# Kernel tuning notes

Hardware: AMD Instinct MI355X
Metric: run time of the kernel (lower is better)

## Reference

```python
import jax, jax.numpy as jnp
import numpy as np

DIM = 192
WH, WW = 8, 8
N = WH * WW
NUM_HEADS = 6
HEAD_DIM = DIM // NUM_HEADS
SCALE = HEAD_DIM ** (-0.5)
B_ = 4096


def _relative_position_index(Wh, Ww):
    coords = np.stack(np.meshgrid(np.arange(Wh), np.arange(Ww), indexing='ij'))  # [2, Wh, Ww]
    cf = coords.reshape(2, -1)                              # [2, N]
    rel = cf[:, :, None] - cf[:, None, :]                   # [2, N, N]
    rel = rel.transpose(1, 2, 0).astype(np.int64)           # [N, N, 2]
    rel[..., 0] += Wh - 1
    rel[..., 1] += Ww - 1
    rel[..., 0] *= 2 * Ww - 1
    return rel.sum(-1)                                      # [N, N]


REL_IDX = jnp.asarray(_relative_position_index(WH, WW))


def setup_inputs() -> dict:
    key = jax.random.key(0)
    ks = jax.random.split(key, 6)
    x = jax.random.normal(ks[0], (B_, N, DIM), dtype=jnp.float32)
    w_qkv = jax.random.normal(ks[1], (3 * DIM, DIM), dtype=jnp.float32) * (DIM ** -0.5)
    b_qkv = jnp.zeros((3 * DIM,), dtype=jnp.float32)
    w_proj = jax.random.normal(ks[2], (DIM, DIM), dtype=jnp.float32) * (DIM ** -0.5)
    b_proj = jnp.zeros((DIM,), dtype=jnp.float32)
    # torch init is zeros; use small noise so the bias path is exercised
    bias_table = jax.random.normal(ks[3], ((2 * WH - 1) * (2 * WW - 1), NUM_HEADS), dtype=jnp.float32) * 0.02
    return {"x": x, "w_qkv": w_qkv, "b_qkv": b_qkv, "w_proj": w_proj,
            "b_proj": b_proj, "bias_table": bias_table}


def reference(x, w_qkv, b_qkv, w_proj, b_proj, bias_table):
    B, n, C = x.shape
    qkv = jnp.einsum('bnc,dc->bnd', x, w_qkv) + b_qkv        # [B, N, 3C]
    qkv = qkv.reshape(B, n, 3, NUM_HEADS, HEAD_DIM)
    q = qkv[:, :, 0].transpose(0, 2, 1, 3) * SCALE            # [B, H, N, hd]
    k = qkv[:, :, 1].transpose(0, 2, 1, 3)
    v = qkv[:, :, 2].transpose(0, 2, 1, 3)
    attn = jnp.einsum('bhnd,bhmd->bhnm', q, k)                # [B, H, N, N]
    bias = bias_table[REL_IDX]                                # [N, N, H]
    attn = attn + bias.transpose(2, 0, 1)[None]               # broadcast over B
    attn = jax.nn.softmax(attn, axis=-1)
    out = jnp.einsum('bhnm,bhmd->bnhd', attn, v).reshape(B, n, C)
    return jnp.einsum('bnc,dc->bnd', out, w_proj) + b_proj
```

## Files before the change

### kernel.cpp

```cpp
#include <hip/hip_runtime.h>

#define TOK 64
#define CDIM 192
#define NH 6
#define HD 32
#define NWAVE 12
#define THREADS 768
#define QSCALE 0.17677669529663687f
#define W16_BYTES ((110592 + 36864) * 2)

typedef _Float16 f16x8 __attribute__((ext_vector_type(8)));
typedef _Float16 f16x4 __attribute__((ext_vector_type(4)));
typedef float f32x4 __attribute__((ext_vector_type(4)));

__device__ __forceinline__ f16x8 ld8(const _Float16* p) {
  return *reinterpret_cast<const f16x8*>(p);
}

__device__ __forceinline__ f16x8 cvt8(const float* __restrict__ p) {
  float4 a = *reinterpret_cast<const float4*>(p);
  float4 c = *reinterpret_cast<const float4*>(p + 4);
  f16x8 r;
  r[0] = (_Float16)a.x; r[1] = (_Float16)a.y; r[2] = (_Float16)a.z; r[3] = (_Float16)a.w;
  r[4] = (_Float16)c.x; r[5] = (_Float16)c.y; r[6] = (_Float16)c.z; r[7] = (_Float16)c.w;
  return r;
}

__global__ void cvt_weights(const float* __restrict__ wq, const float* __restrict__ wp,
                            _Float16* __restrict__ w16) {
  int i = blockIdx.x * 256 + threadIdx.x;
  if (i < 27648) {
    float4 v = reinterpret_cast<const float4*>(wq)[i];
    f16x4 h;
    h[0] = (_Float16)v.x; h[1] = (_Float16)v.y; h[2] = (_Float16)v.z; h[3] = (_Float16)v.w;
    *reinterpret_cast<f16x4*>(w16 + (size_t)i * 4) = h;
  } else if (i < 36864) {
    int j = i - 27648;
    float4 v = reinterpret_cast<const float4*>(wp)[j];
    f16x4 h;
    h[0] = (_Float16)v.x; h[1] = (_Float16)v.y; h[2] = (_Float16)v.z; h[3] = (_Float16)v.w;
    *reinterpret_cast<f16x4*>(w16 + 110592 + (size_t)j * 4) = h;
  }
}

template <bool W16>
__global__ __launch_bounds__(THREADS, 1) void winattn(
    const float* __restrict__ x, const float* __restrict__ w_qkv,
    const float* __restrict__ b_qkv, const float* __restrict__ w_proj,
    const float* __restrict__ b_proj, const float* __restrict__ bias_table,
    const _Float16* __restrict__ w16, float* __restrict__ out) {
  __shared__ __align__(16) _Float16 xob[24 * TOK * 8];
  __shared__ __align__(16) _Float16 qb[NH * 4 * TOK * 8];
  __shared__ __align__(16) _Float16 kb[NH * 4 * TOK * 8];
  __shared__ __align__(16) _Float16 vtb[NH * 8 * HD * 8];
  __shared__ __align__(16) _Float16 pbw[NWAVE * 16 * TOK];
  __shared__ float bias_sm[225 * NH];

  const int tid = threadIdx.x;
  const int w   = tid >> 6;
  const int l   = tid & 63;
  const int l15 = l & 15;
  const int lg  = l >> 4;
  const int b   = blockIdx.x;
  const f32x4 vzero = {0.f, 0.f, 0.f, 0.f};

  const float* xg = x + (size_t)b * (TOK * CDIM);
#pragma unroll
  for (int i = tid; i < TOK * CDIM / 4; i += THREADS) {
    int n = i / (CDIM / 4);
    int c = (i % (CDIM / 4)) * 4;
    float4 v = reinterpret_cast<const float4*>(xg)[i];
    f16x4 h4;
    h4[0] = (_Float16)v.x; h4[1] = (_Float16)v.y;
    h4[2] = (_Float16)v.z; h4[3] = (_Float16)v.w;
    *reinterpret_cast<f16x4*>(&xob[((c >> 3) * TOK + n) * 8 + (c & 7)]) = h4;
  }
  for (int i = tid; i < 225 * NH; i += THREADS) bias_sm[i] = bias_table[i];
  __syncthreads();

  const int h   = w >> 1;
  const int sdl = h * HD + (w & 1) * 16 + l15;
  f32x4 acc[3][4];
#pragma unroll
  for (int p = 0; p < 3; ++p)
#pragma unroll
    for (int mt = 0; mt < 4; ++mt) acc[p][mt] = vzero;

#pragma unroll
  for (int ks = 0; ks < 6; ++ks) {
    f16x8 a[4];
#pragma unroll
    for (int mt = 0; mt < 4; ++mt)
      a[mt] = ld8(&xob[((ks * 4 + lg) * TOK + mt * 16 + l15) * 8]);
#pragma unroll
    for (int p = 0; p < 3; ++p) {
      int row = p * CDIM + sdl;
      f16x8 bf;
      if constexpr (W16) bf = ld8(w16 + (size_t)row * CDIM + ks * 32 + lg * 8);
      else               bf = cvt8(w_qkv + (size_t)row * CDIM + ks * 32 + lg * 8);
#pragma unroll
      for (int mt = 0; mt < 4; ++mt)
        acc[p][mt] = __builtin_amdgcn_mfma_f32_16x16x32_f16(a[mt], bf, acc[p][mt], 0, 0, 0);
    }
  }
  {
    const int hd = (w & 1) * 16 + l15;
    float bq0 = b_qkv[sdl], bq1 = b_qkv[CDIM + sdl], bq2 = b_qkv[2 * CDIM + sdl];
#pragma unroll
    for (int mt = 0; mt < 4; ++mt) {
#pragma unroll
      for (int r = 0; r < 4; ++r) {
        int n = mt * 16 + lg * 4 + r;
        qb[h * 2048 + ((hd >> 3) * TOK + n) * 8 + (hd & 7)] =
            (_Float16)((acc[0][mt][r] + bq0) * QSCALE);
        kb[h * 2048 + ((hd >> 3) * TOK + n) * 8 + (hd & 7)] =
            (_Float16)(acc[1][mt][r] + bq1);
        vtb[h * 2048 + ((n >> 3) * HD + hd) * 8 + (n & 7)] =
            (_Float16)(acc[2][mt][r] + bq2);
      }
    }
  }
  __syncthreads();

  {
    const int pw = w * (16 * TOK);
#pragma unroll
    for (int ii = 0; ii < 2; ++ii) {
      const int it = (w & 1) * 2 + ii;
      f16x8 qf = ld8(&qb[h * 2048 + (lg * TOK + it * 16 + l15) * 8]);
      f32x4 st[4];
#pragma unroll
      for (int jt = 0; jt < 4; ++jt) {
        f16x8 kf = ld8(&kb[h * 2048 + (lg * TOK + jt * 16 + l15) * 8]);
        st[jt] = __builtin_amdgcn_mfma_f32_16x16x32_f16(kf, qf, vzero, 0, 0, 0);
      }
      const int i = it * 16 + l15, yi = i >> 3, xi = i & 7;
#pragma unroll
      for (int jt = 0; jt < 4; ++jt) {
#pragma unroll
        for (int r = 0; r < 4; ++r) {
          int j = jt * 16 + lg * 4 + r, yj = j >> 3, xj = j & 7;
          st[jt][r] += bias_sm[((yi - yj + 7) * 15 + (xi - xj + 7)) * NH + h];
        }
      }
      float m = st[0][0];
#pragma unroll
      for (int jt = 0; jt < 4; ++jt)
#pragma unroll
        for (int r = 0; r < 4; ++r) m = fmaxf(m, st[jt][r]);
      m = fmaxf(m, __shfl_xor(m, 16, 64));
      m = fmaxf(m, __shfl_xor(m, 32, 64));
      float e[4][4], sum = 0.f;
#pragma unroll
      for (int jt = 0; jt < 4; ++jt)
#pragma unroll
        for (int r = 0; r < 4; ++r) { e[jt][r] = __expf(st[jt][r] - m); sum += e[jt][r]; }
      sum += __shfl_xor(sum, 16, 64);
      sum += __shfl_xor(sum, 32, 64);
      float inv = 1.f / sum;
#pragma unroll
      for (int jt = 0; jt < 4; ++jt) {
        f16x4 pk;
#pragma unroll
        for (int r = 0; r < 4; ++r) pk[r] = (_Float16)(e[jt][r] * inv);
        *reinterpret_cast<f16x4*>(
            &pbw[pw + ((jt * 2 + (lg >> 1)) * 16 + l15) * 8 + (lg & 1) * 4]) = pk;
      }
      f32x4 o[2] = {vzero, vzero};
#pragma unroll
      for (int ks = 0; ks < 2; ++ks) {
        f16x8 pf = ld8(&pbw[pw + ((ks * 4 + lg) * 16 + l15) * 8]);
#pragma unroll
        for (int nt = 0; nt < 2; ++nt) {
          f16x8 vf = ld8(&vtb[h * 2048 + ((ks * 4 + lg) * HD + nt * 16 + l15) * 8]);
          o[nt] = __builtin_amdgcn_mfma_f32_16x16x32_f16(pf, vf, o[nt], 0, 0, 0);
        }
      }
#pragma unroll
      for (int nt = 0; nt < 2; ++nt) {
        int c = h * HD + nt * 16 + l15;
#pragma unroll
        for (int r = 0; r < 4; ++r) {
          int i2 = it * 16 + lg * 4 + r;
          xob[((c >> 3) * TOK + i2) * 8 + (c & 7)] = (_Float16)o[nt][r];
        }
      }
    }
  }
  __syncthreads();

  {
    const int e = w * 16 + l15;
    f32x4 pacc[4];
#pragma unroll
    for (int mt = 0; mt < 4; ++mt) pacc[mt] = vzero;
#pragma unroll
    for (int ks = 0; ks < 6; ++ks) {
      f16x8 bf;
      if constexpr (W16) bf = ld8(w16 + 110592 + (size_t)e * CDIM + ks * 32 + lg * 8);
      else               bf = cvt8(w_proj + (size_t)e * CDIM + ks * 32 + lg * 8);
#pragma unroll
      for (int mt = 0; mt < 4; ++mt) {
        f16x8 a = ld8(&xob[((ks * 4 + lg) * TOK + mt * 16 + l15) * 8]);
        pacc[mt] = __builtin_amdgcn_mfma_f32_16x16x32_f16(a, bf, pacc[mt], 0, 0, 0);
      }
    }
    float bp = b_proj[e];
#pragma unroll
    for (int mt = 0; mt < 4; ++mt) {
#pragma unroll
      for (int r = 0; r < 4; ++r) {
        int n = mt * 16 + lg * 4 + r;
        out[((size_t)b * TOK + n) * CDIM + e] = pacc[mt][r] + bp;
      }
    }
  }
}

extern "C" void kernel_launch(void* const* d_in, const int* in_sizes, int n_in,
                              void* d_out, int out_size, void* d_ws, size_t ws_size,
                              hipStream_t stream) {
  const float* x          = (const float*)d_in[0];
  const float* w_qkv      = (const float*)d_in[1];
  const float* b_qkv      = (const float*)d_in[2];
  const float* w_proj     = (const float*)d_in[3];
  const float* b_proj     = (const float*)d_in[4];
  const float* bias_table = (const float*)d_in[5];
  float* out = (float*)d_out;
  int B = in_sizes[0] / (TOK * CDIM);

  if (ws_size >= (size_t)W16_BYTES) {
    _Float16* w16 = (_Float16*)d_ws;
    hipLaunchKernelGGL(cvt_weights, dim3(144), dim3(256), 0, stream, w_qkv, w_proj, w16);
    hipLaunchKernelGGL(winattn<true>, dim3(B), dim3(THREADS), 0, stream,
                       x, w_qkv, b_qkv, w_proj, b_proj, bias_table, w16, out);
  } else {
    hipLaunchKernelGGL(winattn<false>, dim3(B), dim3(THREADS), 0, stream,
                       x, w_qkv, b_qkv, w_proj, b_proj, bias_table,
                       (const _Float16*)nullptr, out);
  }
}
```

Baseline: 266.6 us.

## Halve block to six waves, reuse LDS buffers, precompute per-lane bias layout

The block shrinks from 12 to 6 waves, one wave per head, and launch bounds now request three blocks per CU. LDS drops to three reused 24 KB buffers so more blocks fit. The prep kernel also expands the relative-position bias into a per-lane fp16 layout in workspace, replacing per-element shared-memory gather and index arithmetic with two vector loads. Each wave carries more accumulators (6x4 tiles), which raises register pressure, and an extra barrier is added to allow buffer reuse.

Result: slower. 323.3 us (+21.3%).

```diff
diff --git a/kernel.cpp b/kernel.cpp
--- a/kernel.cpp
+++ b/kernel.cpp
@@ -4,10 +4,15 @@
 #define CDIM 192
 #define NH 6
 #define HD 32
-#define NWAVE 12
-#define THREADS 768
+#define NWAVE 6
+#define THREADS 384
 #define QSCALE 0.17677669529663687f
-#define W16_BYTES ((110592 + 36864) * 2)
+
+#define WQ16_OFF 0
+#define WP16_OFF 110592
+#define BIAS_OFF 147456
+#define WS_HALFS (147456 + 24576)
+#define WS_BYTES (WS_HALFS * 2)
 
 typedef _Float16 f16x8 __attribute__((ext_vector_type(8)));
 typedef _Float16 f16x4 __attribute__((ext_vector_type(4)));
@@ -26,34 +31,42 @@
   return r;
 }
 
-__global__ void cvt_weights(const float* __restrict__ wq, const float* __restrict__ wp,
-                            _Float16* __restrict__ w16) {
+__global__ void prep_ws(const float* __restrict__ wq, const float* __restrict__ wp,
+                        const float* __restrict__ bt, _Float16* __restrict__ ws) {
   int i = blockIdx.x * 256 + threadIdx.x;
   if (i < 27648) {
     float4 v = reinterpret_cast<const float4*>(wq)[i];
     f16x4 h;
     h[0] = (_Float16)v.x; h[1] = (_Float16)v.y; h[2] = (_Float16)v.z; h[3] = (_Float16)v.w;
-    *reinterpret_cast<f16x4*>(w16 + (size_t)i * 4) = h;
+    *reinterpret_cast<f16x4*>(ws + WQ16_OFF + (size_t)i * 4) = h;
   } else if (i < 36864) {
     int j = i - 27648;
     float4 v = reinterpret_cast<const float4*>(wp)[j];
     f16x4 h;
     h[0] = (_Float16)v.x; h[1] = (_Float16)v.y; h[2] = (_Float16)v.z; h[3] = (_Float16)v.w;
-    *reinterpret_cast<f16x4*>(w16 + 110592 + (size_t)j * 4) = h;
-  }
-}
-
-template <bool W16>
-__global__ __launch_bounds__(THREADS, 1) void winattn(
+    *reinterpret_cast<f16x4*>(ws + WP16_OFF + (size_t)j * 4) = h;
+  } else if (i < 61440) {
+    int j = i - 36864;
+    int hit = j >> 10;
+    int l = (j >> 4) & 63;
+    int s = j & 15;
+    int h = hit >> 2, it = hit & 3;
+    int ii = it * 16 + (l & 15);
+    int jj = (s >> 2) * 16 + (l >> 4) * 4 + (s & 3);
+    int rel = ((ii >> 3) - (jj >> 3) + 7) * 15 + ((ii & 7) - (jj & 7) + 7);
+    ws[BIAS_OFF + j] = (_Float16)bt[rel * NH + h];
+  }
+}
+
+template <bool WS>
+__global__ __launch_bounds__(THREADS, 3) void winattn(
     const float* __restrict__ x, const float* __restrict__ w_qkv,
     const float* __restrict__ b_qkv, const float* __restrict__ w_proj,
     const float* __restrict__ b_proj, const float* __restrict__ bias_table,
-    const _Float16* __restrict__ w16, float* __restrict__ out) {
-  __shared__ __align__(16) _Float16 xob[24 * TOK * 8];
-  __shared__ __align__(16) _Float16 qb[NH * 4 * TOK * 8];
-  __shared__ __align__(16) _Float16 kb[NH * 4 * TOK * 8];
-  __shared__ __align__(16) _Float16 vtb[NH * 8 * HD * 8];
-  __shared__ __align__(16) _Float16 pbw[NWAVE * 16 * TOK];
+    const _Float16* __restrict__ ws, float* __restrict__ out) {
+  __shared__ __align__(16) _Float16 Ab[24 * TOK * 8];
+  __shared__ __align__(16) _Float16 Bb[24 * TOK * 8];
+  __shared__ __align__(16) _Float16 Cb[24 * TOK * 8];
   __shared__ float bias_sm[225 * NH];
 
   const int tid = threadIdx.x;
@@ -73,75 +86,107 @@
     f16x4 h4;
     h4[0] = (_Float16)v.x; h4[1] = (_Float16)v.y;
     h4[2] = (_Float16)v.z; h4[3] = (_Float16)v.w;
-    *reinterpret_cast<f16x4*>(&xob[((c >> 3) * TOK + n) * 8 + (c & 7)]) = h4;
-  }
-  for (int i = tid; i < 225 * NH; i += THREADS) bias_sm[i] = bias_table[i];
-  __syncthreads();
-
-  const int h   = w >> 1;
-  const int sdl = h * HD + (w & 1) * 16 + l15;
-  f32x4 acc[3][4];
-#pragma unroll
-  for (int p = 0; p < 3; ++p)
-#pragma unroll
-    for (int mt = 0; mt < 4; ++mt) acc[p][mt] = vzero;
+    *reinterpret_cast<f16x4*>(&Ab[((c >> 3) * TOK + n) * 8 + (c & 7)]) = h4;
+  }
+  if constexpr (!WS) {
+    for (int i = tid; i < 225 * NH; i += THREADS) bias_sm[i] = bias_table[i];
+  }
+  __syncthreads();
+
+  f32x4 acc[6][4];
+#pragma unroll
+  for (int g = 0; g < 6; ++g)
+#pragma unroll
+    for (int mt = 0; mt < 4; ++mt) acc[g][mt] = vzero;
 
 #pragma unroll
   for (int ks = 0; ks < 6; ++ks) {
     f16x8 a[4];
 #pragma unroll
     for (int mt = 0; mt < 4; ++mt)
-      a[mt] = ld8(&xob[((ks * 4 + lg) * TOK + mt * 16 + l15) * 8]);
-#pragma unroll
-    for (int p = 0; p < 3; ++p) {
-      int row = p * CDIM + sdl;
+      a[mt] = ld8(&Ab[((ks * 4 + lg) * TOK + mt * 16 + l15) * 8]);
+#pragma unroll
+    for (int g = 0; g < 6; ++g) {
+      int row = (w + 6 * g) * 16 + l15;
       f16x8 bf;
-      if constexpr (W16) bf = ld8(w16 + (size_t)row * CDIM + ks * 32 + lg * 8);
-      else               bf = cvt8(w_qkv + (size_t)row * CDIM + ks * 32 + lg * 8);
+      if constexpr (WS) bf = ld8(ws + WQ16_OFF + (size_t)row * CDIM + ks * 32 + lg * 8);
+      else              bf = cvt8(w_qkv + (size_t)row * CDIM + ks * 32 + lg * 8);
 #pragma unroll
       for (int mt = 0; mt < 4; ++mt)
-        acc[p][mt] = __builtin_amdgcn_mfma_f32_16x16x32_f16(a[mt], bf, acc[p][mt], 0, 0, 0);
-    }
-  }
-  {
-    const int hd = (w & 1) * 16 + l15;
-    float bq0 = b_qkv[sdl], bq1 = b_qkv[CDIM + sdl], bq2 = b_qkv[2 * CDIM + sdl];
-#pragma unroll
-    for (int mt = 0; mt < 4; ++mt) {
+        acc[g][mt] = __builtin_amdgcn_mfma_f32_16x16x32_f16(a[mt], bf, acc[g][mt], 0, 0, 0);
+    }
+  }
+#pragma unroll
+  for (int g = 0; g < 4; ++g) {
+    int row = (w + 6 * g) * 16 + l15;
+    int dl = row - (g >> 1) * CDIM;
+    int hh = dl >> 5, hd = dl & 31;
+    float bq = b_qkv[row];
+    _Float16* dst = (g < 2) ? Bb : Cb;
+    float scale = (g < 2) ? QSCALE : 1.f;
+#pragma unroll
+    for (int mt = 0; mt < 4; ++mt)
 #pragma unroll
       for (int r = 0; r < 4; ++r) {
         int n = mt * 16 + lg * 4 + r;
-        qb[h * 2048 + ((hd >> 3) * TOK + n) * 8 + (hd & 7)] =
-            (_Float16)((acc[0][mt][r] + bq0) * QSCALE);
-        kb[h * 2048 + ((hd >> 3) * TOK + n) * 8 + (hd & 7)] =
-            (_Float16)(acc[1][mt][r] + bq1);
-        vtb[h * 2048 + ((n >> 3) * HD + hd) * 8 + (n & 7)] =
-            (_Float16)(acc[2][mt][r] + bq2);
-      }
-    }
+        dst[hh * 2048 + ((hd >> 3) * TOK + n) * 8 + (hd & 7)] =
+            (_Float16)((acc[g][mt][r] + bq) * scale);
+      }
+  }
+  __syncthreads();
+#pragma unroll
+  for (int g = 4; g < 6; ++g) {
+    int row = (w + 6 * g) * 16 + l15;
+    int dl = row - 2 * CDIM;
+    int hh = dl >> 5, hd = dl & 31;
+    float bq = b_qkv[row];
+#pragma unroll
+    for (int mt = 0; mt < 4; ++mt)
+#pragma unroll
+      for (int r = 0; r < 4; ++r) {
+        int n = mt * 16 + lg * 4 + r;
+        Ab[hh * 2048 + ((n >> 3) * HD + hd) * 8 + (n & 7)] = (_Float16)(acc[g][mt][r] + bq);
+      }
   }
   __syncthreads();
 
   {
-    const int pw = w * (16 * TOK);
-#pragma unroll
-    for (int ii = 0; ii < 2; ++ii) {
-      const int it = (w & 1) * 2 + ii;
-      f16x8 qf = ld8(&qb[h * 2048 + (lg * TOK + it * 16 + l15) * 8]);
+    f16x8 qf[4], kf[4], vf[4];
+#pragma unroll
+    for (int it = 0; it < 4; ++it)
+      qf[it] = ld8(&Bb[w * 2048 + (lg * TOK + it * 16 + l15) * 8]);
+#pragma unroll
+    for (int jt = 0; jt < 4; ++jt)
+      kf[jt] = ld8(&Cb[w * 2048 + (lg * TOK + jt * 16 + l15) * 8]);
+#pragma unroll
+    for (int z = 0; z < 4; ++z) {
+      int ks = z >> 1, nt = z & 1;
+      vf[z] = ld8(&Ab[w * 2048 + ((ks * 4 + lg) * HD + nt * 16 + l15) * 8]);
+    }
+
+#pragma unroll
+    for (int it = 0; it < 4; ++it) {
       f32x4 st[4];
 #pragma unroll
-      for (int jt = 0; jt < 4; ++jt) {
-        f16x8 kf = ld8(&kb[h * 2048 + (lg * TOK + jt * 16 + l15) * 8]);
-        st[jt] = __builtin_amdgcn_mfma_f32_16x16x32_f16(kf, qf, vzero, 0, 0, 0);
-      }
-      const int i = it * 16 + l15, yi = i >> 3, xi = i & 7;
-#pragma unroll
-      for (int jt = 0; jt < 4; ++jt) {
-#pragma unroll
-        for (int r = 0; r < 4; ++r) {
-          int j = jt * 16 + lg * 4 + r, yj = j >> 3, xj = j & 7;
-          st[jt][r] += bias_sm[((yi - yj + 7) * 15 + (xi - xj + 7)) * NH + h];
-        }
+      for (int jt = 0; jt < 4; ++jt)
+        st[jt] = __builtin_amdgcn_mfma_f32_16x16x32_f16(kf[jt], qf[it], vzero, 0, 0, 0);
+      if constexpr (WS) {
+        const _Float16* bw = ws + BIAS_OFF + ((w * 4 + it) * 64 + l) * 16;
+        f16x8 b0 = ld8(bw), b1 = ld8(bw + 8);
+#pragma unroll
+        for (int jt = 0; jt < 4; ++jt)
+#pragma unroll
+          for (int r = 0; r < 4; ++r)
+            st[jt][r] += (float)((jt < 2) ? b0[jt * 4 + r] : b1[(jt - 2) * 4 + r]);
+      } else {
+        int i = it * 16 + l15, yi = i >> 3, xi = i & 7;
+#pragma unroll
+        for (int jt = 0; jt < 4; ++jt)
+#pragma unroll
+          for (int r = 0; r < 4; ++r) {
+            int j = jt * 16 + lg * 4 + r, yj = j >> 3, xj = j & 7;
+            st[jt][r] += bias_sm[((yi - yj + 7) * 15 + (xi - xj + 7)) * NH + w];
+          }
       }
       float m = st[0][0];
 #pragma unroll
@@ -158,31 +203,30 @@
       sum += __shfl_xor(sum, 16, 64);
       sum += __shfl_xor(sum, 32, 64);
       float inv = 1.f / sum;
+      _Float16* pbase = &Bb[w * 2048 + (it & 1) * 1024];
 #pragma unroll
       for (int jt = 0; jt < 4; ++jt) {
         f16x4 pk;
 #pragma unroll
         for (int r = 0; r < 4; ++r) pk[r] = (_Float16)(e[jt][r] * inv);
         *reinterpret_cast<f16x4*>(
-            &pbw[pw + ((jt * 2 + (lg >> 1)) * 16 + l15) * 8 + (lg & 1) * 4]) = pk;
+            &pbase[((jt * 2 + (lg >> 1)) * 16 + l15) * 8 + (lg & 1) * 4]) = pk;
       }
       f32x4 o[2] = {vzero, vzero};
 #pragma unroll
       for (int ks = 0; ks < 2; ++ks) {
-        f16x8 pf = ld8(&pbw[pw + ((ks * 4 + lg) * 16 + l15) * 8]);
-#pragma unroll
-        for (int nt = 0; nt < 2; ++nt) {
-          f16x8 vf = ld8(&vtb[h * 2048 + ((ks * 4 + lg) * HD + nt * 16 + l15) * 8]);
-          o[nt] = __builtin_amdgcn_mfma_f32_16x16x32_f16(pf, vf, o[nt], 0, 0, 0);
-        }
+        f16x8 pf = ld8(&pbase[((ks * 4 + lg) * 16 + l15) * 8]);
+#pragma unroll
+        for (int nt = 0; nt < 2; ++nt)
+          o[nt] = __builtin_amdgcn_mfma_f32_16x16x32_f16(pf, vf[ks * 2 + nt], o[nt], 0, 0, 0);
       }
 #pragma unroll
       for (int nt = 0; nt < 2; ++nt) {
-        int c = h * HD + nt * 16 + l15;
+        int c = w * HD + nt * 16 + l15;
 #pragma unroll
         for (int r = 0; r < 4; ++r) {
           int i2 = it * 16 + lg * 4 + r;
-          xob[((c >> 3) * TOK + i2) * 8 + (c & 7)] = (_Float16)o[nt][r];
+          Cb[((c >> 3) * TOK + i2) * 8 + (c & 7)] = (_Float16)o[nt][r];
         }
       }
     }
@@ -190,29 +234,39 @@
   __syncthreads();
 
   {
-    const int e = w * 16 + l15;
-    f32x4 pacc[4];
-#pragma unroll
-    for (int mt = 0; mt < 4; ++mt) pacc[mt] = vzero;
+    f32x4 pacc[2][4];
+#pragma unroll
+    for (int g = 0; g < 2; ++g)
+#pragma unroll
+      for (int mt = 0; mt < 4; ++mt) pacc[g][mt] = vzero;
 #pragma unroll
     for (int ks = 0; ks < 6; ++ks) {
-      f16x8 bf;
-      if constexpr (W16) bf = ld8(w16 + 110592 + (size_t)e * CDIM + ks * 32 + lg * 8);
-      else               bf = cvt8(w_proj + (size_t)e * CDIM + ks * 32 + lg * 8);
-#pragma unroll
-      for (int mt = 0; mt < 4; ++mt) {
-        f16x8 a = ld8(&xob[((ks * 4 + lg) * TOK + mt * 16 + l15) * 8]);
-        pacc[mt] = __builtin_amdgcn_mfma_f32_16x16x32_f16(a, bf, pacc[mt], 0, 0, 0);
-      }
-    }
-    float bp = b_proj[e];
-#pragma unroll
-    for (int mt = 0; mt < 4; ++mt) {
-#pragma unroll
-      for (int r = 0; r < 4; ++r) {
-        int n = mt * 16 + lg * 4 + r;
-        out[((size_t)b * TOK + n) * CDIM + e] = pacc[mt][r] + bp;
-      }
+      f16x8 a[4];
+#pragma unroll
+      for (int mt = 0; mt < 4; ++mt)
+        a[mt] = ld8(&Cb[((ks * 4 + lg) * TOK + mt * 16 + l15) * 8]);
+#pragma unroll
+      for (int g = 0; g < 2; ++g) {
+        int e = (w + 6 * g) * 16 + l15;
+        f16x8 bf;
+        if constexpr (WS) bf = ld8(ws + WP16_OFF + (size_t)e * CDIM + ks * 32 + lg * 8);
+        else              bf = cvt8(w_proj + (size_t)e * CDIM + ks * 32 + lg * 8);
+#pragma unroll
+        for (int mt = 0; mt < 4; ++mt)
+          pacc[g][mt] = __builtin_amdgcn_mfma_f32_16x16x32_f16(a[mt], bf, pacc[g][mt], 0, 0, 0);
+      }
+    }
+#pragma unroll
+    for (int g = 0; g < 2; ++g) {
+      int e = (w + 6 * g) * 16 + l15;
+      float bp = b_proj[e];
+#pragma unroll
+      for (int mt = 0; mt < 4; ++mt)
+#pragma unroll
+        for (int r = 0; r < 4; ++r) {
+          int n = mt * 16 + lg * 4 + r;
+          out[((size_t)b * TOK + n) * CDIM + e] = pacc[g][mt][r] + bp;
+        }
     }
   }
 }
@@ -229,11 +283,12 @@
   float* out = (float*)d_out;
   int B = in_sizes[0] / (TOK * CDIM);
 
-  if (ws_size >= (size_t)W16_BYTES) {
-    _Float16* w16 = (_Float16*)d_ws;
-    hipLaunchKernelGGL(cvt_weights, dim3(144), dim3(256), 0, stream, w_qkv, w_proj, w16);
+  if (ws_size >= (size_t)WS_BYTES) {
+    _Float16* ws = (_Float16*)d_ws;
+    hipLaunchKernelGGL(prep_ws, dim3(240), dim3(256), 0, stream,
+                       w_qkv, w_proj, bias_table, ws);
     hipLaunchKernelGGL(winattn<true>, dim3(B), dim3(THREADS), 0, stream,
-                       x, w_qkv, b_qkv, w_proj, b_proj, bias_table, w16, out);
+                       x, w_qkv, b_qkv, w_proj, b_proj, bias_table, ws, out);
   } else {
     hipLaunchKernelGGL(winattn<false>, dim3(B), dim3(THREADS), 0, stream,
                        x, w_qkv, b_qkv, w_proj, b_proj, bias_table,
```
